# Kernel optimization log

Measured on AMD Instinct MI355X. Metric: run time of the kernel, lower is better.

## Reference

```python
import jax, jax.numpy as jnp
import numpy as np

B, L, C, N = 8, 1024, 1024, 5000


def setup_inputs() -> dict:
    key = jax.random.key(0)
    k1, k2, k3 = jax.random.split(key, 3)
    z = jax.random.normal(k1, (B, L, C), dtype=jnp.float32)
    codebook = jax.random.normal(k2, (N, C), dtype=jnp.float32)
    mask = jax.random.bernoulli(k3, 0.9, (B, L))  # bool [B, L]
    return {"z": z, "mask": mask, "codebook": codebook}


def reference(z, mask, codebook):
    # pairwise squared L2 distance via the GEMM identity:
    # ||z - c||^2 = ||z||^2 + ||c||^2 - 2 z.c   (same math as broadcast-subtract-square-sum)
    z2 = jnp.sum(z * z, axis=-1, keepdims=True)        # [B, L, 1]
    c2 = jnp.sum(codebook * codebook, axis=-1)         # [N]
    cross = jnp.einsum('blc,nc->bln', z, codebook)     # [B, L, N]
    distance = z2 + c2 - 2.0 * cross                   # [B, L, N]
    indices = jnp.argmin(distance, axis=-1)            # [B, L] int
    quantized = codebook[indices]                      # gather -> [B, L, C]
    quantized = jnp.where(mask[..., None], quantized, 0.0)  # quantized[~mask] = 0
    commit_loss = jnp.float32(0.0)
    return quantized, indices, commit_loss
```

## Files before the change

### kernel.cpp

```cpp
#include <hip/hip_runtime.h>
#include <stdint.h>


#define M_TOTAL 8192
#define K_DIM   1024
#define N_REAL  5000
#define N_PAD   5120

typedef __attribute__((ext_vector_type(8))) short bf16x8;
typedef __attribute__((ext_vector_type(4))) float f32x4;

__device__ __forceinline__ ushort f2bf(float x) {
  union { float f; uint32_t u; } v; v.f = x;
  uint32_t r = v.u + 0x7FFFu + ((v.u >> 16) & 1u);
  return (ushort)(r >> 16);
}

__device__ __forceinline__ void async16(void* lds, const void* g) {
  __builtin_amdgcn_global_load_lds(
      (const __attribute__((address_space(1))) void*)g,
      (__attribute__((address_space(3))) void*)lds, 16, 0, 0);
}


__global__ __launch_bounds__(256) void convert_z(const float4* __restrict__ z4,
                                                 ushort* __restrict__ zb, int n4) {
  int i = blockIdx.x * blockDim.x + threadIdx.x;
  int stride = gridDim.x * blockDim.x;
  for (; i < n4; i += stride) {
    float4 v = z4[i];
    ushort4 u;
    u.x = f2bf(v.x); u.y = f2bf(v.y); u.z = f2bf(v.z); u.w = f2bf(v.w);
    *(ushort4*)&zb[(size_t)i * 4] = u;
  }
}

__global__ __launch_bounds__(256) void prep_cb(const float* __restrict__ cb,
                                               ushort* __restrict__ cbb,
                                               float* __restrict__ c2) {
  __shared__ float sred[4];
  const int row = blockIdx.x;
  const int tid = threadIdx.x;
  if (row >= N_REAL) {
    ushort4 zz; zz.x = zz.y = zz.z = zz.w = 0;
    *(ushort4*)&cbb[(size_t)row * K_DIM + tid * 4] = zz;
    if (tid == 0) c2[row] = 0.f;
    return;
  }
  float4 v = ((const float4*)(cb + (size_t)row * K_DIM))[tid];
  ushort4 u;
  u.x = f2bf(v.x); u.y = f2bf(v.y); u.z = f2bf(v.z); u.w = f2bf(v.w);
  *(ushort4*)&cbb[(size_t)row * K_DIM + tid * 4] = u;
  float s = v.x * v.x + v.y * v.y + v.z * v.z + v.w * v.w;
  #pragma unroll
  for (int off = 32; off; off >>= 1) s += __shfl_down(s, off);
  int wv = tid >> 6, ln = tid & 63;
  if (ln == 0) sred[wv] = s;
  __syncthreads();
  if (tid == 0) c2[row] = sred[0] + sred[1] + sred[2] + sred[3];
}


__global__ __launch_bounds__(256) void gemm_score(const ushort* __restrict__ A,
                                                  const ushort* __restrict__ Bm,
                                                  const float* __restrict__ c2,
                                                  float* __restrict__ dist,
                                                  int rowBase) {
  __shared__ ushort sA[128 * 64];
  __shared__ ushort sB[128 * 64];
  const int tid  = threadIdx.x;
  const int wave = tid >> 6, lane = tid & 63;
  const int wm = wave >> 1, wn = wave & 1;
  const int tM = rowBase + blockIdx.y * 128;
  const int tN = blockIdx.x * 128;

  f32x4 acc[4][4];
  #pragma unroll
  for (int i = 0; i < 4; ++i)
    #pragma unroll
    for (int j = 0; j < 4; ++j)
      acc[i][j] = (f32x4)0.f;

  char* sAb = (char*)sA;
  char* sBb = (char*)sB;
  const int o = tid * 16;

  for (int k0 = 0; k0 < K_DIM; k0 += 64) {
    __syncthreads();
    #pragma unroll
    for (int it = 0; it < 4; ++it) {
      int ob = o + it * 4096;
      int r  = ob >> 7;
      int cbyte = ob & 127;
      const char* ga = (const char*)A + ((size_t)(tM + r) * K_DIM + k0) * 2 + cbyte;
      async16(sAb + ob, ga);
      const char* gb = (const char*)Bm + ((size_t)(tN + r) * K_DIM + k0) * 2 + cbyte;
      async16(sBb + ob, gb);
    }
    __syncthreads();
    #pragma unroll
    for (int kk = 0; kk < 2; ++kk) {
      bf16x8 af[4], bfr[4];
      const int kcol = kk * 32 + (lane >> 4) * 8;
      #pragma unroll
      for (int f = 0; f < 4; ++f) {
        int ra = wm * 64 + f * 16 + (lane & 15);
        af[f]  = *(const bf16x8*)&sA[ra * 64 + kcol];
        int rb = wn * 64 + f * 16 + (lane & 15);
        bfr[f] = *(const bf16x8*)&sB[rb * 64 + kcol];
      }
      #pragma unroll
      for (int i = 0; i < 4; ++i)
        #pragma unroll
        for (int j = 0; j < 4; ++j)
          acc[i][j] = __builtin_amdgcn_mfma_f32_16x16x32_bf16(af[i], bfr[j], acc[i][j], 0, 0, 0);
    }
  }

  const int cl = lane & 15, rg = lane >> 4;
  const int mBaseLocal = blockIdx.y * 128 + wm * 64;
  #pragma unroll
  for (int j = 0; j < 4; ++j) {
    int n = tN + wn * 64 + j * 16 + cl;
    float c2n = c2[n];
    #pragma unroll
    for (int i = 0; i < 4; ++i) {
      #pragma unroll
      for (int r = 0; r < 4; ++r) {
        int m = mBaseLocal + i * 16 + rg * 4 + r;
        dist[(size_t)m * N_PAD + n] = c2n - 2.0f * acc[i][j][r];
      }
    }
  }
}


__global__ __launch_bounds__(256) void argmin_gather(const float* __restrict__ dist,
                                                     const float* __restrict__ z,
                                                     const float* __restrict__ cb,
                                                     const int* __restrict__ mask,
                                                     float* __restrict__ out_q,
                                                     float* __restrict__ out_i,
                                                     float* __restrict__ out_loss,
                                                     int rowBase) {
  __shared__ __align__(16) float srow[N_REAL];
  __shared__ float swv[4];
  __shared__ int   swi[4];
  __shared__ float sminv;
  __shared__ int   scand[64];
  __shared__ int   scnt;
  __shared__ double sdv[4];
  __shared__ double sbestd;
  __shared__ int    sbesti;

  const int tid = threadIdx.x;
  const int ml  = blockIdx.x;
  const int mg  = rowBase + ml;
  const float* row = dist + (size_t)ml * N_PAD;

  float bestv = 3.4e38f; int besti = 0x7fffffff;
  for (int i = tid; i < N_REAL / 4; i += 256) {
    float4 v = ((const float4*)row)[i];
    ((float4*)srow)[i] = v;
    int b = i * 4;
    if (v.x < bestv) { bestv = v.x; besti = b; }
    if (v.y < bestv) { bestv = v.y; besti = b + 1; }
    if (v.z < bestv) { bestv = v.z; besti = b + 2; }
    if (v.w < bestv) { bestv = v.w; besti = b + 3; }
  }
  #pragma unroll
  for (int off = 32; off; off >>= 1) {
    float ov = __shfl_down(bestv, off);
    int   oi = __shfl_down(besti, off);
    if (ov < bestv || (ov == bestv && oi < besti)) { bestv = ov; besti = oi; }
  }
  const int wv = tid >> 6, ln = tid & 63;
  if (ln == 0) { swv[wv] = bestv; swi[wv] = besti; }
  __syncthreads();
  if (tid == 0) {
    float bv = swv[0]; int bi = swi[0];
    for (int w = 1; w < 4; ++w)
      if (swv[w] < bv || (swv[w] == bv && swi[w] < bi)) { bv = swv[w]; bi = swi[w]; }
    sminv = bv; scnt = 0;
  }
  __syncthreads();

  const float thr = sminv + 8.0f;
  for (int i = tid; i < N_REAL; i += 256) {
    if (srow[i] <= thr) {
      int p = atomicAdd(&scnt, 1);
      if (p < 64) scand[p] = i;
    }
  }
  __syncthreads();
  int nc = scnt < 64 ? scnt : 64;

  if (tid == 0) { sbestd = 1e300; sbesti = 0x7fffffff; }
  __syncthreads();
  const float* zr = z + (size_t)mg * K_DIM;
  for (int c = 0; c < nc; ++c) {
    int n = scand[c];
    const float* cr = cb + (size_t)n * K_DIM;
    float4 cv = ((const float4*)cr)[tid];
    float4 zv = ((const float4*)zr)[tid];
    double lsum = (double)cv.x * ((double)cv.x - 2.0 * (double)zv.x)
                + (double)cv.y * ((double)cv.y - 2.0 * (double)zv.y)
                + (double)cv.z * ((double)cv.z - 2.0 * (double)zv.z)
                + (double)cv.w * ((double)cv.w - 2.0 * (double)zv.w);
    #pragma unroll
    for (int off = 32; off; off >>= 1) lsum += __shfl_down(lsum, off);
    if (ln == 0) sdv[wv] = lsum;
    __syncthreads();
    if (tid == 0) {
      double s = sdv[0] + sdv[1] + sdv[2] + sdv[3];
      if (s < sbestd || (s == sbestd && n < sbesti)) { sbestd = s; sbesti = n; }
    }
    __syncthreads();
  }

  const int bidx = sbesti;
  if (tid == 0) out_i[mg] = (float)bidx;
  const int mk = mask[mg];
  float4 qz; qz.x = qz.y = qz.z = qz.w = 0.f;
  float4 src = ((const float4*)(cb + (size_t)bidx * K_DIM))[tid];
  ((float4*)(out_q + (size_t)mg * K_DIM))[tid] = mk ? src : qz;
  if (mg == 0 && tid == 0) *out_loss = 0.0f;
}


extern "C" void kernel_launch(void* const* d_in, const int* in_sizes, int n_in,
                              void* d_out, int out_size, void* d_ws, size_t ws_size,
                              hipStream_t stream) {
  const float* z    = (const float*)d_in[0];
  const int*   mask = (const int*)d_in[1];
  const float* cb   = (const float*)d_in[2];

  float* out      = (float*)d_out;
  float* out_q    = out;
  float* out_i    = out + (size_t)M_TOTAL * K_DIM;
  float* out_loss = out_i + M_TOTAL;

  char* ws = (char*)d_ws;
  ushort* zb   = (ushort*)(ws);
  ushort* cbb  = (ushort*)(ws + 16777216);
  float*  c2   = (float*)(ws + 27262976);
  float*  dist = (float*)(ws + 27283456);

  const size_t fixed = 27283456;
  size_t avail = (ws_size > fixed) ? (ws_size - fixed) : 0;
  long long cmax = (long long)(avail / ((size_t)N_PAD * 4));
  int chunkM = (int)((cmax / 128) * 128);
  if (chunkM > M_TOTAL) chunkM = M_TOTAL;
  if (chunkM < 128) chunkM = 128;

  convert_z<<<2048, 256, 0, stream>>>((const float4*)z, zb, (M_TOTAL * K_DIM) / 4);
  prep_cb<<<N_PAD, 256, 0, stream>>>(cb, cbb, c2);

  for (int cs = 0; cs < M_TOTAL; cs += chunkM) {
    int cm = (chunkM < M_TOTAL - cs) ? chunkM : (M_TOTAL - cs);
    dim3 g(N_PAD / 128, cm / 128);
    gemm_score<<<g, 256, 0, stream>>>(zb, cbb, c2, dist, cs);
    argmin_gather<<<cm, 256, 0, stream>>>(dist, z, cb, mask, out_q, out_i, out_loss, cs);
  }
}
```

Before: 288.2 us.

## Fuse argmin into GEMM epilogue with atomic min and candidate lists

Removes the full [M, N] distance matrix write and re-read. The GEMM epilogue now reduces each tile row to a local minimum, publishes it through a 64-bit atomicMin on a packed (ordered-float, index) key, and appends near-minimum candidates to a per-row list. A finalize kernel rescores those candidates in double precision and gathers the chosen codebook row. This saves roughly 160 MB of HBM traffic and drops the chunking loop. In exchange it adds global atomics in the epilogue and makes candidate capture depend on the order in which tiles finish.

```diff
diff --git a/kernel.cpp b/kernel.cpp
--- a/kernel.cpp
+++ b/kernel.cpp
@@ -2,10 +2,12 @@
 #include <stdint.h>
 
 
-#define M_TOTAL 8192
-#define K_DIM   1024
-#define N_REAL  5000
-#define N_PAD   5120
+#define M_TOTAL  8192
+#define K_DIM    1024
+#define N_REAL   5000
+#define N_PAD    5120
+#define CAND_CAP 256
+#define MARGIN   8.0f
 
 typedef __attribute__((ext_vector_type(8))) short bf16x8;
 typedef __attribute__((ext_vector_type(4))) float f32x4;
@@ -22,6 +24,23 @@
       (__attribute__((address_space(3))) void*)lds, 16, 0, 0);
 }
 
+__device__ __forceinline__ uint32_t fenc(float f) {
+  union { float f; uint32_t u; } v; v.f = f;
+  return v.u ^ ((v.u >> 31) ? 0xFFFFFFFFu : 0x80000000u);
+}
+__device__ __forceinline__ float fdec(uint32_t e) {
+  uint32_t u = e ^ ((e & 0x80000000u) ? 0x80000000u : 0xFFFFFFFFu);
+  union { uint32_t u; float f; } v; v.u = u; return v.f;
+}
+
+
+__global__ __launch_bounds__(256) void init_state(unsigned long long* __restrict__ gmin,
+                                                  int* __restrict__ ccnt,
+                                                  float* __restrict__ out_loss) {
+  int i = blockIdx.x * blockDim.x + threadIdx.x;
+  if (i < M_TOTAL) { gmin[i] = ~0ull; ccnt[i] = 0; }
+  if (i == 0) out_loss[0] = 0.0f;
+}
 
 __global__ __launch_bounds__(256) void convert_z(const float4* __restrict__ z4,
                                                  ushort* __restrict__ zb, int n4) {
@@ -64,14 +83,15 @@
 __global__ __launch_bounds__(256) void gemm_score(const ushort* __restrict__ A,
                                                   const ushort* __restrict__ Bm,
                                                   const float* __restrict__ c2,
-                                                  float* __restrict__ dist,
-                                                  int rowBase) {
+                                                  unsigned long long* __restrict__ gmin,
+                                                  int* __restrict__ ccnt,
+                                                  unsigned long long* __restrict__ cand) {
   __shared__ ushort sA[128 * 64];
   __shared__ ushort sB[128 * 64];
   const int tid  = threadIdx.x;
   const int wave = tid >> 6, lane = tid & 63;
   const int wm = wave >> 1, wn = wave & 1;
-  const int tM = rowBase + blockIdx.y * 128;
+  const int tM = blockIdx.y * 128;
   const int tN = blockIdx.x * 128;
 
   f32x4 acc[4][4];
@@ -118,91 +138,103 @@
   }
 
   const int cl = lane & 15, rg = lane >> 4;
-  const int mBaseLocal = blockIdx.y * 128 + wm * 64;
+  int   ncol[4];
+  float c2v[4];
   #pragma unroll
   for (int j = 0; j < 4; ++j) {
-    int n = tN + wn * 64 + j * 16 + cl;
-    float c2n = c2[n];
-    #pragma unroll
-    for (int i = 0; i < 4; ++i) {
-      #pragma unroll
-      for (int r = 0; r < 4; ++r) {
-        int m = mBaseLocal + i * 16 + rg * 4 + r;
-        dist[(size_t)m * N_PAD + n] = c2n - 2.0f * acc[i][j][r];
-      }
-    }
-  }
-}
-
-
-__global__ __launch_bounds__(256) void argmin_gather(const float* __restrict__ dist,
-                                                     const float* __restrict__ z,
-                                                     const float* __restrict__ cb,
-                                                     const int* __restrict__ mask,
-                                                     float* __restrict__ out_q,
-                                                     float* __restrict__ out_i,
-                                                     float* __restrict__ out_loss,
-                                                     int rowBase) {
-  __shared__ __align__(16) float srow[N_REAL];
-  __shared__ float swv[4];
-  __shared__ int   swi[4];
-  __shared__ float sminv;
-  __shared__ int   scand[64];
-  __shared__ int   scnt;
+    ncol[j] = tN + wn * 64 + j * 16 + cl;
+    c2v[j]  = (ncol[j] < N_REAL) ? c2[ncol[j]] : 0.f;
+  }
+
+  #pragma unroll
+  for (int i = 0; i < 4; ++i) {
+    #pragma unroll
+    for (int r = 0; r < 4; ++r) {
+      const int m = tM + wm * 64 + i * 16 + rg * 4 + r;
+      float sc[4];
+      float bv = 3.4e38f; int bc = 0x7fffffff;
+      #pragma unroll
+      for (int j = 0; j < 4; ++j) {
+        sc[j] = (ncol[j] < N_REAL) ? (c2v[j] - 2.0f * acc[i][j][r]) : 3.4e38f;
+        if (sc[j] < bv || (sc[j] == bv && ncol[j] < bc)) { bv = sc[j]; bc = ncol[j]; }
+      }
+      #pragma unroll
+      for (int off = 1; off < 16; off <<= 1) {
+        float ov = __shfl_xor(bv, off);
+        int   oc = __shfl_xor(bc, off);
+        if (ov < bv || (ov == bv && oc < bc)) { bv = ov; bc = oc; }
+      }
+      unsigned long long cur = gmin[m];
+      float gv = 3.4e38f;
+      if (cur != ~0ull) gv = fdec((uint32_t)(cur >> 32));
+      const float thr = fminf(bv, gv) + MARGIN;
+      #pragma unroll
+      for (int j = 0; j < 4; ++j) {
+        if (ncol[j] < N_REAL && sc[j] <= thr) {
+          int p = atomicAdd(&ccnt[m], 1);
+          if (p < CAND_CAP) {
+            union { float f; uint32_t u; } s; s.f = sc[j];
+            cand[(size_t)m * CAND_CAP + p] = ((unsigned long long)(uint32_t)ncol[j] << 32) | s.u;
+          }
+        }
+      }
+      if (cl == 0 && bc != 0x7fffffff) {
+        unsigned long long pk = ((unsigned long long)fenc(bv) << 32) | (uint32_t)bc;
+        atomicMin(&gmin[m], pk);
+      }
+    }
+  }
+}
+
+
+__global__ __launch_bounds__(256) void finalize(const unsigned long long* __restrict__ gmin,
+                                                const int* __restrict__ ccnt,
+                                                const unsigned long long* __restrict__ cand,
+                                                const float* __restrict__ z,
+                                                const float* __restrict__ cb,
+                                                const int* __restrict__ mask,
+                                                float* __restrict__ out_q,
+                                                float* __restrict__ out_i) {
+  __shared__ int scand[CAND_CAP];
+  __shared__ int scnt;
   __shared__ double sdv[4];
   __shared__ double sbestd;
   __shared__ int    sbesti;
 
   const int tid = threadIdx.x;
-  const int ml  = blockIdx.x;
-  const int mg  = rowBase + ml;
-  const float* row = dist + (size_t)ml * N_PAD;
-
-  float bestv = 3.4e38f; int besti = 0x7fffffff;
-  for (int i = tid; i < N_REAL / 4; i += 256) {
-    float4 v = ((const float4*)row)[i];
-    ((float4*)srow)[i] = v;
-    int b = i * 4;
-    if (v.x < bestv) { bestv = v.x; besti = b; }
-    if (v.y < bestv) { bestv = v.y; besti = b + 1; }
-    if (v.z < bestv) { bestv = v.z; besti = b + 2; }
-    if (v.w < bestv) { bestv = v.w; besti = b + 3; }
-  }
-  #pragma unroll
-  for (int off = 32; off; off >>= 1) {
-    float ov = __shfl_down(bestv, off);
-    int   oi = __shfl_down(besti, off);
-    if (ov < bestv || (ov == bestv && oi < besti)) { bestv = ov; besti = oi; }
-  }
+  const int m   = blockIdx.x;
+
+  const unsigned long long g = gmin[m];
+  const float gv   = fdec((uint32_t)(g >> 32));
+  const int   gcol = (int)(g & 0xFFFFFFFFu);
+  int cnt = ccnt[m]; if (cnt > CAND_CAP) cnt = CAND_CAP;
+
+  if (tid == 0) { scand[0] = gcol; scnt = 1; }
+  __syncthreads();
+
+  const float thr = gv + MARGIN;
+  for (int i = tid; i < cnt; i += 256) {
+    unsigned long long e = cand[(size_t)m * CAND_CAP + i];
+    union { uint32_t u; float f; } s; s.u = (uint32_t)(e & 0xFFFFFFFFu);
+    int col = (int)(e >> 32);
+    if (col != gcol && s.f <= thr) {
+      int p = atomicAdd(&scnt, 1);
+      if (p < CAND_CAP) scand[p] = col;
+    }
+  }
+  __syncthreads();
+  int nc = scnt; if (nc > CAND_CAP) nc = CAND_CAP;
+
+  if (tid == 0) { sbestd = 1e300; sbesti = 0x7fffffff; }
+  __syncthreads();
+
   const int wv = tid >> 6, ln = tid & 63;
-  if (ln == 0) { swv[wv] = bestv; swi[wv] = besti; }
-  __syncthreads();
-  if (tid == 0) {
-    float bv = swv[0]; int bi = swi[0];
-    for (int w = 1; w < 4; ++w)
-      if (swv[w] < bv || (swv[w] == bv && swi[w] < bi)) { bv = swv[w]; bi = swi[w]; }
-    sminv = bv; scnt = 0;
-  }
-  __syncthreads();
-
-  const float thr = sminv + 8.0f;
-  for (int i = tid; i < N_REAL; i += 256) {
-    if (srow[i] <= thr) {
-      int p = atomicAdd(&scnt, 1);
-      if (p < 64) scand[p] = i;
-    }
-  }
-  __syncthreads();
-  int nc = scnt < 64 ? scnt : 64;
-
-  if (tid == 0) { sbestd = 1e300; sbesti = 0x7fffffff; }
-  __syncthreads();
-  const float* zr = z + (size_t)mg * K_DIM;
+  const float* zr = z + (size_t)m * K_DIM;
+  const float4 zv = ((const float4*)zr)[tid];
+
   for (int c = 0; c < nc; ++c) {
-    int n = scand[c];
-    const float* cr = cb + (size_t)n * K_DIM;
-    float4 cv = ((const float4*)cr)[tid];
-    float4 zv = ((const float4*)zr)[tid];
+    const int n = scand[c];
+    float4 cv = ((const float4*)(cb + (size_t)n * K_DIM))[tid];
     double lsum = (double)cv.x * ((double)cv.x - 2.0 * (double)zv.x)
                 + (double)cv.y * ((double)cv.y - 2.0 * (double)zv.y)
                 + (double)cv.z * ((double)cv.z - 2.0 * (double)zv.z)
@@ -219,12 +251,11 @@
   }
 
   const int bidx = sbesti;
-  if (tid == 0) out_i[mg] = (float)bidx;
-  const int mk = mask[mg];
+  if (tid == 0) out_i[m] = (float)bidx;
+  const int mk = mask[m];
   float4 qz; qz.x = qz.y = qz.z = qz.w = 0.f;
   float4 src = ((const float4*)(cb + (size_t)bidx * K_DIM))[tid];
-  ((float4*)(out_q + (size_t)mg * K_DIM))[tid] = mk ? src : qz;
-  if (mg == 0 && tid == 0) *out_loss = 0.0f;
+  ((float4*)(out_q + (size_t)m * K_DIM))[tid] = mk ? src : qz;
 }
 
 
@@ -241,25 +272,18 @@
   float* out_loss = out_i + M_TOTAL;
 
   char* ws = (char*)d_ws;
-  ushort* zb   = (ushort*)(ws);
-  ushort* cbb  = (ushort*)(ws + 16777216);
-  float*  c2   = (float*)(ws + 27262976);
-  float*  dist = (float*)(ws + 27283456);
-
-  const size_t fixed = 27283456;
-  size_t avail = (ws_size > fixed) ? (ws_size - fixed) : 0;
-  long long cmax = (long long)(avail / ((size_t)N_PAD * 4));
-  int chunkM = (int)((cmax / 128) * 128);
-  if (chunkM > M_TOTAL) chunkM = M_TOTAL;
-  if (chunkM < 128) chunkM = 128;
-
+  ushort*             zb   = (ushort*)(ws);
+  ushort*             cbb  = (ushort*)(ws + 16777216);
+  float*              c2   = (float*)(ws + 27262976);
+  unsigned long long* gmin = (unsigned long long*)(ws + 27283456);
+  int*                ccnt = (int*)(ws + 27348992);
+  unsigned long long* cand = (unsigned long long*)(ws + 27381760);
+
+  init_state<<<32, 256, 0, stream>>>(gmin, ccnt, out_loss);
   convert_z<<<2048, 256, 0, stream>>>((const float4*)z, zb, (M_TOTAL * K_DIM) / 4);
   prep_cb<<<N_PAD, 256, 0, stream>>>(cb, cbb, c2);
 
-  for (int cs = 0; cs < M_TOTAL; cs += chunkM) {
-    int cm = (chunkM < M_TOTAL - cs) ? chunkM : (M_TOTAL - cs);
-    dim3 g(N_PAD / 128, cm / 128);
-    gemm_score<<<g, 256, 0, stream>>>(zb, cbb, c2, dist, cs);
-    argmin_gather<<<cm, 256, 0, stream>>>(dist, z, cb, mask, out_q, out_i, out_loss, cs);
-  }
-}
+  dim3 g(N_PAD / 128, M_TOTAL / 128);
+  gemm_score<<<g, 256, 0, stream>>>(zb, cbb, c2, gmin, ccnt, cand);
+  finalize<<<M_TOTAL, 256, 0, stream>>>(gmin, ccnt, cand, z, cb, mask, out_q, out_i);
+}
```

New measurement: 500.8 us. 73.8% more time.
